# Performance work log

Measured on AMD Instinct MI355X. Metric: run time of the kernel, lower is better.

Reference implementation:

```python
import jax, jax.numpy as jnp
import numpy as np

B, D, H, E = 4096, 256, 1024, 8


def setup_inputs() -> dict:
    key = jax.random.key(0)
    k_x, k_w1, k_b1, k_w2, k_b2, k_idx = jax.random.split(key, 6)
    return {
        "x": jax.random.normal(k_x, (B, D), dtype=jnp.float32),
        "W1": jax.random.normal(k_w1, (E, D, H), dtype=jnp.float32) * (1.0 / np.sqrt(D)),
        "b1": jax.random.normal(k_b1, (E, H), dtype=jnp.float32) * 0.01,
        "W2": jax.random.normal(k_w2, (E, H, D), dtype=jnp.float32) * (1.0 / np.sqrt(H)),
        "b2": jax.random.normal(k_b2, (E, D), dtype=jnp.float32) * 0.01,
        "expert_idx": jax.random.randint(k_idx, (B,), 0, E, dtype=jnp.int64)
        if jax.config.jax_enable_x64 else jax.random.randint(k_idx, (B,), 0, E, dtype=jnp.int32),
    }


def reference(x, W1, b1, W2, b2, expert_idx):
    # Each sample i is routed to expert expert_idx[i] (= video_id_to_index lookup),
    # runs the expert MLP on its batch-of-1 row, and results are concatenated.
    # Vectorized as: run all experts over the batch, combine with a one-hot mask.
    E_ = W1.shape[0]
    onehot = jax.nn.one_hot(expert_idx, E_, dtype=x.dtype)          # [B, E]
    h = jax.nn.relu(jnp.einsum("bd,edh->ebh", x, W1) + b1[:, None, :])  # [E, B, H]
    y = jnp.einsum("ebh,ehd->ebd", h, W2) + b2[:, None, :]              # [E, B, D]
    return jnp.einsum("be,ebd->bd", onehot, y)                           # [B, D]
```

## Files before the change

kernel.cpp:

```cpp
#include <hip/hip_runtime.h>


#define D_DIM 256
#define H_DIM 1024
#define E_NUM 8
#define B_TOK 4096
#define CAP   1024

typedef __attribute__((ext_vector_type(8))) short short8;
typedef __attribute__((ext_vector_type(4))) float f32x4;
typedef unsigned short u16;
typedef unsigned int u32;
typedef unsigned long long u64;

#define CNT_OFF    0
#define BUCKET_OFF 1024
#define XG_OFF     (BUCKET_OFF + E_NUM*B_TOK*4)
#define W1T_OFF    (XG_OFF  + (size_t)E_NUM*CAP*D_DIM*2)
#define W2T_OFF    (W1T_OFF + (size_t)E_NUM*H_DIM*D_DIM*2)
#define HW_OFF     (W2T_OFF + (size_t)E_NUM*D_DIM*H_DIM*2)

__device__ __forceinline__ u16 f2bf(float f) {
    u32 u = __builtin_bit_cast(u32, f);
    u = (u + 0x7fffu + ((u >> 16) & 1u)) >> 16;
    return (u16)u;
}

__global__ __launch_bounds__(1024) void bin_kernel(const int* __restrict__ eidx,
                                                   int* __restrict__ cnt,
                                                   int* __restrict__ bucket) {
    __shared__ int wsum[16], wbase[16];
    __shared__ int base, chunk_total;
    const int e = blockIdx.x, tid = threadIdx.x;
    const int lane = tid & 63, wv = tid >> 6;
    if (tid == 0) base = 0;
    __syncthreads();
    #pragma unroll
    for (int c = 0; c < 4; ++c) {
        int t = c * 1024 + tid;
        bool m = (eidx[t] == e);
        u64 bal = __ballot(m);
        int pfx = __popcll(bal & ((1ull << lane) - 1ull));
        if (lane == 0) wsum[wv] = __popcll(bal);
        __syncthreads();
        if (tid == 0) {
            int s = 0;
            #pragma unroll
            for (int i = 0; i < 16; ++i) { wbase[i] = s; s += wsum[i]; }
            chunk_total = s;
        }
        __syncthreads();
        if (m) bucket[e * B_TOK + base + wbase[wv] + pfx] = t;
        __syncthreads();
        if (tid == 0) base += chunk_total;
        __syncthreads();
    }
    if (tid == 0) cnt[e] = base;
}

__device__ __forceinline__ void trans64(const float* __restrict__ in,
                                        u16* __restrict__ outp,
                                        int R, int C, int rt, int ct,
                                        int tt, u16* tile) {
    #pragma unroll
    for (int it = 0; it < 4; ++it) {
        int r = it * 16 + (tt >> 4);
        int c4 = (tt & 15) * 4;
        float4 v = *(const float4*)(in + (size_t)(rt * 64 + r) * C + ct * 64 + c4);
        u64 pk = (u64)f2bf(v.x) | ((u64)f2bf(v.y) << 16)
               | ((u64)f2bf(v.z) << 32) | ((u64)f2bf(v.w) << 48);
        *(u64*)&tile[r * 68 + c4] = pk;
    }
    __syncthreads();
    #pragma unroll
    for (int it = 0; it < 2; ++it) {
        int oc = it * 32 + (tt >> 3);
        int r0 = (tt & 7) * 8;
        u32 p0 = tile[(r0 + 0) * 68 + oc] | ((u32)tile[(r0 + 1) * 68 + oc] << 16);
        u32 p1 = tile[(r0 + 2) * 68 + oc] | ((u32)tile[(r0 + 3) * 68 + oc] << 16);
        u32 p2 = tile[(r0 + 4) * 68 + oc] | ((u32)tile[(r0 + 5) * 68 + oc] << 16);
        u32 p3 = tile[(r0 + 6) * 68 + oc] | ((u32)tile[(r0 + 7) * 68 + oc] << 16);
        *(uint4*)(outp + (size_t)(ct * 64 + oc) * R + rt * 64 + r0) = uint4{p0, p1, p2, p3};
    }
}

__global__ __launch_bounds__(256) void prep_kernel(
    const float* __restrict__ x, const float* __restrict__ W1,
    const float* __restrict__ W2, const int* __restrict__ cnt,
    const int* __restrict__ bucket, u16* __restrict__ xg,
    u16* __restrict__ w1t, u16* __restrict__ w2t)
{
    __shared__ u16 tile[64 * 68];
    const int b = blockIdx.x, tid = threadIdx.x;
    if (b < 512) {
        int e = b >> 6, tj = b & 63;
        trans64(W1 + (size_t)e * D_DIM * H_DIM, w1t + (size_t)e * H_DIM * D_DIM,
                D_DIM, H_DIM, tj >> 4, tj & 15, tid, tile);
    } else if (b < 1024) {
        int e = (b - 512) >> 6, tj = (b - 512) & 63;
        trans64(W2 + (size_t)e * H_DIM * D_DIM, w2t + (size_t)e * D_DIM * H_DIM,
                H_DIM, D_DIM, tj >> 2, tj & 3, tid, tile);
    } else {
        int gb = b - 1024;
        int wv = tid >> 6, lane = tid & 63;
        #pragma unroll
        for (int i = 0; i < 4; ++i) {
            int row = gb * 16 + wv * 4 + i;
            int e = row >> 10, pos = row & (CAP - 1);
            int n = min(cnt[e], CAP);
            u64 pk = 0;
            if (pos < n) {
                int tk = bucket[e * B_TOK + pos];
                float4 v = *(const float4*)(x + (size_t)tk * D_DIM + lane * 4);
                pk = (u64)f2bf(v.x) | ((u64)f2bf(v.y) << 16)
                   | ((u64)f2bf(v.z) << 32) | ((u64)f2bf(v.w) << 48);
            }
            *(u64*)&xg[(size_t)row * D_DIM + lane * 4] = pk;
        }
    }
}

__global__ __launch_bounds__(256, 2) void gemm1_kernel(
    const u16* __restrict__ xg, const u16* __restrict__ w1t,
    const float* __restrict__ b1, const int* __restrict__ cnt,
    u16* __restrict__ hw)
{
    __shared__ u16 xs[64 * 264];
    __shared__ u16 w1s[64 * 264];
    __shared__ u16 hs[64 * 72];

    int b = blockIdx.x;
    int e = b >> 8, tile = (b >> 4) & 15, hch = b & 15;
    int n = min(cnt[e], CAP);
    if (tile * 64 >= n) return;

    int tid = threadIdx.x;
    int w = tid >> 6, L = tid & 63, l15 = L & 15, l4 = L >> 4;
    int wr = (w >> 1) * 32, wc = (w & 1) * 32;

    {
        const u16* gx = xg + ((size_t)e * CAP + tile * 64) * D_DIM;
        const u16* gw = w1t + ((size_t)e * H_DIM + hch * 64) * D_DIM;
        int rr = tid >> 5, cc = (tid & 31) * 8;
        #pragma unroll
        for (int it = 0; it < 8; ++it) {
            int row = it * 8 + rr;
            *(short8*)&xs[row * 264 + cc]  = *(const short8*)&gx[(size_t)row * D_DIM + cc];
            *(short8*)&w1s[row * 264 + cc] = *(const short8*)&gw[(size_t)row * D_DIM + cc];
        }
    }
    __syncthreads();

    f32x4 acc[2][2];
    #pragma unroll
    for (int i = 0; i < 2; ++i)
        #pragma unroll
        for (int j = 0; j < 2; ++j) acc[i][j] = (f32x4){0.f, 0.f, 0.f, 0.f};

    #pragma unroll
    for (int k = 0; k < 8; ++k) {
        short8 a0 = *(const short8*)&xs[(wr + l15) * 264 + k * 32 + l4 * 8];
        short8 a1 = *(const short8*)&xs[(wr + 16 + l15) * 264 + k * 32 + l4 * 8];
        short8 b0 = *(const short8*)&w1s[(wc + l15) * 264 + k * 32 + l4 * 8];
        short8 b1v = *(const short8*)&w1s[(wc + 16 + l15) * 264 + k * 32 + l4 * 8];
        acc[0][0] = __builtin_amdgcn_mfma_f32_16x16x32_bf16(a0, b0, acc[0][0], 0, 0, 0);
        acc[0][1] = __builtin_amdgcn_mfma_f32_16x16x32_bf16(a0, b1v, acc[0][1], 0, 0, 0);
        acc[1][0] = __builtin_amdgcn_mfma_f32_16x16x32_bf16(a1, b0, acc[1][0], 0, 0, 0);
        acc[1][1] = __builtin_amdgcn_mfma_f32_16x16x32_bf16(a1, b1v, acc[1][1], 0, 0, 0);
    }

    #pragma unroll
    for (int mr = 0; mr < 2; ++mr)
        #pragma unroll
        for (int nc = 0; nc < 2; ++nc) {
            float bias = b1[e * H_DIM + hch * 64 + wc + nc * 16 + l15];
            #pragma unroll
            for (int j = 0; j < 4; ++j) {
                float v = acc[mr][nc][j] + bias;
                v = fmaxf(v, 0.f);
                hs[(wr + mr * 16 + l4 * 4 + j) * 72 + wc + nc * 16 + l15] = f2bf(v);
            }
        }
    __syncthreads();
    {
        u16* gh = hw + ((size_t)e * CAP + tile * 64) * H_DIM + hch * 64;
        int rr8 = tid >> 3, off = (tid & 7) * 8;
        #pragma unroll
        for (int it = 0; it < 2; ++it) {
            int row = it * 32 + rr8;
            *(short8*)&gh[(size_t)row * H_DIM + off] = *(const short8*)&hs[row * 72 + off];
        }
    }
}

__global__ __launch_bounds__(256, 2) void gemm2_kernel(
    const u16* __restrict__ hw, const u16* __restrict__ w2t,
    const float* __restrict__ b2, const int* __restrict__ cnt,
    const int* __restrict__ bucket, float* __restrict__ out)
{
    __shared__ u16 as_[64 * 264];
    __shared__ u16 bs[64 * 264];

    int b = blockIdx.x;
    int e = b >> 6, tile = (b >> 2) & 15, nch = b & 3;
    int n = min(cnt[e], CAP);
    if (tile * 64 >= n) return;

    int tid = threadIdx.x;
    int w = tid >> 6, L = tid & 63, l15 = L & 15, l4 = L >> 4;
    int wr = (w >> 1) * 32, wc = (w & 1) * 32;

    f32x4 acc[2][2];
    #pragma unroll
    for (int i = 0; i < 2; ++i)
        #pragma unroll
        for (int j = 0; j < 2; ++j) acc[i][j] = (f32x4){0.f, 0.f, 0.f, 0.f};

    const u16* ga = hw + ((size_t)e * CAP + tile * 64) * H_DIM;
    const u16* gb = w2t + ((size_t)e * D_DIM + nch * 64) * H_DIM;

    for (int kc = 0; kc < 4; ++kc) {
        __syncthreads();
        int rr = tid >> 5, cc = (tid & 31) * 8;
        #pragma unroll
        for (int it = 0; it < 8; ++it) {
            int row = it * 8 + rr;
            *(short8*)&as_[row * 264 + cc] = *(const short8*)&ga[(size_t)row * H_DIM + kc * 256 + cc];
            *(short8*)&bs[row * 264 + cc]  = *(const short8*)&gb[(size_t)row * H_DIM + kc * 256 + cc];
        }
        __syncthreads();
        #pragma unroll
        for (int k = 0; k < 8; ++k) {
            short8 a0 = *(const short8*)&as_[(wr + l15) * 264 + k * 32 + l4 * 8];
            short8 a1 = *(const short8*)&as_[(wr + 16 + l15) * 264 + k * 32 + l4 * 8];
            short8 b0 = *(const short8*)&bs[(wc + l15) * 264 + k * 32 + l4 * 8];
            short8 b1v = *(const short8*)&bs[(wc + 16 + l15) * 264 + k * 32 + l4 * 8];
            acc[0][0] = __builtin_amdgcn_mfma_f32_16x16x32_bf16(a0, b0, acc[0][0], 0, 0, 0);
            acc[0][1] = __builtin_amdgcn_mfma_f32_16x16x32_bf16(a0, b1v, acc[0][1], 0, 0, 0);
            acc[1][0] = __builtin_amdgcn_mfma_f32_16x16x32_bf16(a1, b0, acc[1][0], 0, 0, 0);
            acc[1][1] = __builtin_amdgcn_mfma_f32_16x16x32_bf16(a1, b1v, acc[1][1], 0, 0, 0);
        }
    }

    #pragma unroll
    for (int mr = 0; mr < 2; ++mr)
        #pragma unroll
        for (int jj = 0; jj < 4; ++jj) {
            int m = wr + mr * 16 + l4 * 4 + jj;
            if (tile * 64 + m < n) {
                int token = bucket[e * B_TOK + tile * 64 + m];
                #pragma unroll
                for (int nc = 0; nc < 2; ++nc) {
                    int d = nch * 64 + wc + nc * 16 + l15;
                    out[(size_t)token * D_DIM + d] = acc[mr][nc][jj] + b2[e * D_DIM + d];
                }
            }
        }
}

extern "C" void kernel_launch(void* const* d_in, const int* in_sizes, int n_in,
                              void* d_out, int out_size, void* d_ws, size_t ws_size,
                              hipStream_t stream) {
    const float* x  = (const float*)d_in[0];
    const float* W1 = (const float*)d_in[1];
    const float* b1 = (const float*)d_in[2];
    const float* W2 = (const float*)d_in[3];
    const float* b2 = (const float*)d_in[4];
    const int* eidx = (const int*)d_in[5];
    float* out = (float*)d_out;

    char* ws = (char*)d_ws;
    int* cnt    = (int*)(ws + CNT_OFF);
    int* bucket = (int*)(ws + BUCKET_OFF);
    u16* xg     = (u16*)(ws + XG_OFF);
    u16* w1t    = (u16*)(ws + W1T_OFF);
    u16* w2t    = (u16*)(ws + W2T_OFF);
    u16* hw     = (u16*)(ws + HW_OFF);

    bin_kernel<<<E_NUM, 1024, 0, stream>>>(eidx, cnt, bucket);
    prep_kernel<<<1536, 256, 0, stream>>>(x, W1, W2, cnt, bucket, xg, w1t, w2t);
    gemm1_kernel<<<E_NUM * 16 * 16, 256, 0, stream>>>(xg, w1t, b1, cnt, hw);
    gemm2_kernel<<<E_NUM * 16 * 4, 256, 0, stream>>>(hw, w2t, b2, cnt, bucket, out);
}
```

Before: 40.10 us.

## Fuse binning into prep and gather x directly inside gemm1

Drops the separate binning kernel and folds expert binning into the prep kernel as 8 extra blocks. Removes the xg staging buffer: gemm1 now gathers token rows from x through the bucket, converts them to bf16 in shared memory, and reuses that tile across two hidden chunks per block, which halves the gemm1 grid. The goal is fewer launches and less global traffic. In exchange there is less parallelism in gemm1, the binning runs serially over 16 chunks, and gemm1 does scattered fp32 gather loads.

Measured after the change: 50.29 us. 25.4% more time.

```diff
diff --git a/kernel.cpp b/kernel.cpp
--- a/kernel.cpp
+++ b/kernel.cpp
@@ -15,8 +15,7 @@
 
 #define CNT_OFF    0
 #define BUCKET_OFF 1024
-#define XG_OFF     (BUCKET_OFF + E_NUM*B_TOK*4)
-#define W1T_OFF    (XG_OFF  + (size_t)E_NUM*CAP*D_DIM*2)
+#define W1T_OFF    (BUCKET_OFF + E_NUM*B_TOK*4)
 #define W2T_OFF    (W1T_OFF + (size_t)E_NUM*H_DIM*D_DIM*2)
 #define HW_OFF     (W2T_OFF + (size_t)E_NUM*D_DIM*H_DIM*2)
 
@@ -24,38 +23,6 @@
     u32 u = __builtin_bit_cast(u32, f);
     u = (u + 0x7fffu + ((u >> 16) & 1u)) >> 16;
     return (u16)u;
-}
-
-__global__ __launch_bounds__(1024) void bin_kernel(const int* __restrict__ eidx,
-                                                   int* __restrict__ cnt,
-                                                   int* __restrict__ bucket) {
-    __shared__ int wsum[16], wbase[16];
-    __shared__ int base, chunk_total;
-    const int e = blockIdx.x, tid = threadIdx.x;
-    const int lane = tid & 63, wv = tid >> 6;
-    if (tid == 0) base = 0;
-    __syncthreads();
-    #pragma unroll
-    for (int c = 0; c < 4; ++c) {
-        int t = c * 1024 + tid;
-        bool m = (eidx[t] == e);
-        u64 bal = __ballot(m);
-        int pfx = __popcll(bal & ((1ull << lane) - 1ull));
-        if (lane == 0) wsum[wv] = __popcll(bal);
-        __syncthreads();
-        if (tid == 0) {
-            int s = 0;
-            #pragma unroll
-            for (int i = 0; i < 16; ++i) { wbase[i] = s; s += wsum[i]; }
-            chunk_total = s;
-        }
-        __syncthreads();
-        if (m) bucket[e * B_TOK + base + wbase[wv] + pfx] = t;
-        __syncthreads();
-        if (tid == 0) base += chunk_total;
-        __syncthreads();
-    }
-    if (tid == 0) cnt[e] = base;
 }
 
 __device__ __forceinline__ void trans64(const float* __restrict__ in,
@@ -85,9 +52,9 @@
 }
 
 __global__ __launch_bounds__(256) void prep_kernel(
-    const float* __restrict__ x, const float* __restrict__ W1,
-    const float* __restrict__ W2, const int* __restrict__ cnt,
-    const int* __restrict__ bucket, u16* __restrict__ xg,
+    const float* __restrict__ W1, const float* __restrict__ W2,
+    const int* __restrict__ eidx,
+    int* __restrict__ cnt, int* __restrict__ bucket,
     u16* __restrict__ w1t, u16* __restrict__ w2t)
 {
     __shared__ u16 tile[64 * 68];
@@ -101,94 +68,120 @@
         trans64(W2 + (size_t)e * H_DIM * D_DIM, w2t + (size_t)e * D_DIM * H_DIM,
                 H_DIM, D_DIM, tj >> 2, tj & 3, tid, tile);
     } else {
-        int gb = b - 1024;
-        int wv = tid >> 6, lane = tid & 63;
-        #pragma unroll
-        for (int i = 0; i < 4; ++i) {
-            int row = gb * 16 + wv * 4 + i;
-            int e = row >> 10, pos = row & (CAP - 1);
-            int n = min(cnt[e], CAP);
-            u64 pk = 0;
-            if (pos < n) {
-                int tk = bucket[e * B_TOK + pos];
-                float4 v = *(const float4*)(x + (size_t)tk * D_DIM + lane * 4);
-                pk = (u64)f2bf(v.x) | ((u64)f2bf(v.y) << 16)
-                   | ((u64)f2bf(v.z) << 32) | ((u64)f2bf(v.w) << 48);
-            }
-            *(u64*)&xg[(size_t)row * D_DIM + lane * 4] = pk;
-        }
+        __shared__ int wsum[4];
+        const int e = b - 1024;
+        const int lane = tid & 63, wv = tid >> 6;
+        int base = 0;
+        #pragma unroll
+        for (int c = 0; c < 16; ++c) {
+            int t = c * 256 + tid;
+            bool m = (eidx[t] == e);
+            u64 bal = __ballot(m);
+            int pfx = __popcll(bal & ((1ull << lane) - 1ull));
+            if (lane == 0) wsum[wv] = __popcll(bal);
+            __syncthreads();
+            int wb = 0, total = 0;
+            #pragma unroll
+            for (int i = 0; i < 4; ++i) { if (i < wv) wb += wsum[i]; total += wsum[i]; }
+            if (m) bucket[e * B_TOK + base + wb + pfx] = t;
+            base += total;
+            __syncthreads();
+        }
+        if (tid == 0) cnt[e] = base;
     }
 }
 
 __global__ __launch_bounds__(256, 2) void gemm1_kernel(
-    const u16* __restrict__ xg, const u16* __restrict__ w1t,
+    const float* __restrict__ x, const u16* __restrict__ w1t,
     const float* __restrict__ b1, const int* __restrict__ cnt,
-    u16* __restrict__ hw)
+    const int* __restrict__ bucket, u16* __restrict__ hw)
 {
     __shared__ u16 xs[64 * 264];
     __shared__ u16 w1s[64 * 264];
     __shared__ u16 hs[64 * 72];
 
-    int b = blockIdx.x;
-    int e = b >> 8, tile = (b >> 4) & 15, hch = b & 15;
-    int n = min(cnt[e], CAP);
-    if (tile * 64 >= n) return;
-
-    int tid = threadIdx.x;
-    int w = tid >> 6, L = tid & 63, l15 = L & 15, l4 = L >> 4;
-    int wr = (w >> 1) * 32, wc = (w & 1) * 32;
+    const int b = blockIdx.x;
+    const int e = b >> 7, t = (b >> 3) & 15, hp = b & 7;
+    const int n = min(cnt[e], CAP);
+    const int row0 = t * 64;
+    if (row0 >= n) return;
+
+    const int tid = threadIdx.x;
+    const int w = tid >> 6, L = tid & 63, l15 = L & 15, l4 = L >> 4;
+    const int wr = (w >> 1) * 32, wc = (w & 1) * 32;
 
     {
-        const u16* gx = xg + ((size_t)e * CAP + tile * 64) * D_DIM;
-        const u16* gw = w1t + ((size_t)e * H_DIM + hch * 64) * D_DIM;
-        int rr = tid >> 5, cc = (tid & 31) * 8;
-        #pragma unroll
-        for (int it = 0; it < 8; ++it) {
-            int row = it * 8 + rr;
-            *(short8*)&xs[row * 264 + cc]  = *(const short8*)&gx[(size_t)row * D_DIM + cc];
-            *(short8*)&w1s[row * 264 + cc] = *(const short8*)&gw[(size_t)row * D_DIM + cc];
-        }
-    }
-    __syncthreads();
-
-    f32x4 acc[2][2];
-    #pragma unroll
-    for (int i = 0; i < 2; ++i)
-        #pragma unroll
-        for (int j = 0; j < 2; ++j) acc[i][j] = (f32x4){0.f, 0.f, 0.f, 0.f};
-
-    #pragma unroll
-    for (int k = 0; k < 8; ++k) {
-        short8 a0 = *(const short8*)&xs[(wr + l15) * 264 + k * 32 + l4 * 8];
-        short8 a1 = *(const short8*)&xs[(wr + 16 + l15) * 264 + k * 32 + l4 * 8];
-        short8 b0 = *(const short8*)&w1s[(wc + l15) * 264 + k * 32 + l4 * 8];
-        short8 b1v = *(const short8*)&w1s[(wc + 16 + l15) * 264 + k * 32 + l4 * 8];
-        acc[0][0] = __builtin_amdgcn_mfma_f32_16x16x32_bf16(a0, b0, acc[0][0], 0, 0, 0);
-        acc[0][1] = __builtin_amdgcn_mfma_f32_16x16x32_bf16(a0, b1v, acc[0][1], 0, 0, 0);
-        acc[1][0] = __builtin_amdgcn_mfma_f32_16x16x32_bf16(a1, b0, acc[1][0], 0, 0, 0);
-        acc[1][1] = __builtin_amdgcn_mfma_f32_16x16x32_bf16(a1, b1v, acc[1][1], 0, 0, 0);
-    }
-
-    #pragma unroll
-    for (int mr = 0; mr < 2; ++mr)
-        #pragma unroll
-        for (int nc = 0; nc < 2; ++nc) {
-            float bias = b1[e * H_DIM + hch * 64 + wc + nc * 16 + l15];
-            #pragma unroll
-            for (int j = 0; j < 4; ++j) {
-                float v = acc[mr][nc][j] + bias;
-                v = fmaxf(v, 0.f);
-                hs[(wr + mr * 16 + l4 * 4 + j) * 72 + wc + nc * 16 + l15] = f2bf(v);
-            }
-        }
-    __syncthreads();
-    {
-        u16* gh = hw + ((size_t)e * CAP + tile * 64) * H_DIM + hch * 64;
-        int rr8 = tid >> 3, off = (tid & 7) * 8;
-        #pragma unroll
-        for (int it = 0; it < 2; ++it) {
-            int row = it * 32 + rr8;
-            *(short8*)&gh[(size_t)row * H_DIM + off] = *(const short8*)&hs[row * 72 + off];
+        const int l16 = tid & 15;
+        #pragma unroll
+        for (int rr = 0; rr < 4; ++rr) {
+            int row = rr * 16 + (tid >> 4);
+            bool valid = (row0 + row) < n;
+            int token = valid ? bucket[e * B_TOK + row0 + row] : 0;
+            const float* src = x + (size_t)token * D_DIM + l16 * 4;
+            #pragma unroll
+            for (int i = 0; i < 4; ++i) {
+                float4 v = valid ? *(const float4*)(src + i * 64)
+                                 : float4{0.f, 0.f, 0.f, 0.f};
+                u64 pk = (u64)f2bf(v.x) | ((u64)f2bf(v.y) << 16)
+                       | ((u64)f2bf(v.z) << 32) | ((u64)f2bf(v.w) << 48);
+                *(u64*)&xs[row * 264 + l16 * 4 + i * 64] = pk;
+            }
+        }
+    }
+
+    for (int j = 0; j < 2; ++j) {
+        const int hch = hp * 2 + j;
+        {
+            const u16* gw = w1t + ((size_t)e * H_DIM + hch * 64) * D_DIM;
+            int rr = tid >> 5, cc = (tid & 31) * 8;
+            #pragma unroll
+            for (int it = 0; it < 8; ++it) {
+                int row = it * 8 + rr;
+                *(short8*)&w1s[row * 264 + cc] = *(const short8*)&gw[(size_t)row * D_DIM + cc];
+            }
+        }
+        __syncthreads();
+
+        f32x4 acc[2][2];
+        #pragma unroll
+        for (int i = 0; i < 2; ++i)
+            #pragma unroll
+            for (int jj = 0; jj < 2; ++jj) acc[i][jj] = (f32x4){0.f, 0.f, 0.f, 0.f};
+
+        #pragma unroll
+        for (int k = 0; k < 8; ++k) {
+            short8 a0 = *(const short8*)&xs[(wr + l15) * 264 + k * 32 + l4 * 8];
+            short8 a1 = *(const short8*)&xs[(wr + 16 + l15) * 264 + k * 32 + l4 * 8];
+            short8 b0 = *(const short8*)&w1s[(wc + l15) * 264 + k * 32 + l4 * 8];
+            short8 b1v = *(const short8*)&w1s[(wc + 16 + l15) * 264 + k * 32 + l4 * 8];
+            acc[0][0] = __builtin_amdgcn_mfma_f32_16x16x32_bf16(a0, b0, acc[0][0], 0, 0, 0);
+            acc[0][1] = __builtin_amdgcn_mfma_f32_16x16x32_bf16(a0, b1v, acc[0][1], 0, 0, 0);
+            acc[1][0] = __builtin_amdgcn_mfma_f32_16x16x32_bf16(a1, b0, acc[1][0], 0, 0, 0);
+            acc[1][1] = __builtin_amdgcn_mfma_f32_16x16x32_bf16(a1, b1v, acc[1][1], 0, 0, 0);
+        }
+
+        #pragma unroll
+        for (int mr = 0; mr < 2; ++mr)
+            #pragma unroll
+            for (int nc = 0; nc < 2; ++nc) {
+                float bias = b1[e * H_DIM + hch * 64 + wc + nc * 16 + l15];
+                #pragma unroll
+                for (int jj = 0; jj < 4; ++jj) {
+                    float v = acc[mr][nc][jj] + bias;
+                    v = fmaxf(v, 0.f);
+                    hs[(wr + mr * 16 + l4 * 4 + jj) * 72 + wc + nc * 16 + l15] = f2bf(v);
+                }
+            }
+        __syncthreads();
+
+        {
+            u16* gh = hw + ((size_t)e * CAP + row0) * H_DIM + hch * 64;
+            int rr8 = tid >> 3, off = (tid & 7) * 8;
+            #pragma unroll
+            for (int it = 0; it < 2; ++it) {
+                int row = it * 32 + rr8;
+                *(short8*)&gh[(size_t)row * H_DIM + off] = *(const short8*)&hs[row * 72 + off];
+            }
         }
     }
 }
@@ -272,13 +265,11 @@
     char* ws = (char*)d_ws;
     int* cnt    = (int*)(ws + CNT_OFF);
     int* bucket = (int*)(ws + BUCKET_OFF);
-    u16* xg     = (u16*)(ws + XG_OFF);
     u16* w1t    = (u16*)(ws + W1T_OFF);
     u16* w2t    = (u16*)(ws + W2T_OFF);
     u16* hw     = (u16*)(ws + HW_OFF);
 
-    bin_kernel<<<E_NUM, 1024, 0, stream>>>(eidx, cnt, bucket);
-    prep_kernel<<<1536, 256, 0, stream>>>(x, W1, W2, cnt, bucket, xg, w1t, w2t);
-    gemm1_kernel<<<E_NUM * 16 * 16, 256, 0, stream>>>(xg, w1t, b1, cnt, hw);
+    prep_kernel<<<1032, 256, 0, stream>>>(W1, W2, eidx, cnt, bucket, w1t, w2t);
+    gemm1_kernel<<<E_NUM * 16 * 8, 256, 0, stream>>>(x, w1t, b1, cnt, bucket, hw);
     gemm2_kernel<<<E_NUM * 16 * 4, 256, 0, stream>>>(hw, w2t, b2, cnt, bucket, out);
 }
```
